# Performance work log

Hardware: AMD Instinct MI355X
Metric: run time of the kernel (lower is better)

The kernel has to match this reference:

```python
import jax, jax.numpy as jnp
import numpy as np

N = 100000   # nodes
E = 1000000  # edges
F_IN = 64    # num_node_features
H = 64       # hidden_channels
G = 64       # graphs in batch
OUT = 1


def setup_inputs() -> dict:
    key = jax.random.key(0)
    ks = jax.random.split(key, 16)
    inp = {}
    inp['x'] = jax.random.normal(ks[0], (N, F_IN), dtype=jnp.float32)
    inp['edge_index'] = jax.random.randint(ks[1], (2, E), 0, N, dtype=jnp.int64)
    inp['batch'] = jnp.sort(jax.random.randint(ks[2], (N,), 0, G, dtype=jnp.int64))
    s_in = 1.0 / np.sqrt(F_IN)
    s_h = 1.0 / np.sqrt(H)
    # GraphConv 1: in=F_IN -> H  (lin_rel has bias, lin_root has no bias)
    inp['W1r'] = jax.random.uniform(ks[3], (F_IN, H), jnp.float32, -s_in, s_in)
    inp['b1'] = jax.random.uniform(ks[4], (H,), jnp.float32, -s_in, s_in)
    inp['W1o'] = jax.random.uniform(ks[5], (F_IN, H), jnp.float32, -s_in, s_in)
    # GraphConv 2, 3: H -> H
    inp['W2r'] = jax.random.uniform(ks[6], (H, H), jnp.float32, -s_h, s_h)
    inp['b2'] = jax.random.uniform(ks[7], (H,), jnp.float32, -s_h, s_h)
    inp['W2o'] = jax.random.uniform(ks[8], (H, H), jnp.float32, -s_h, s_h)
    inp['W3r'] = jax.random.uniform(ks[9], (H, H), jnp.float32, -s_h, s_h)
    inp['b3'] = jax.random.uniform(ks[10], (H,), jnp.float32, -s_h, s_h)
    inp['W3o'] = jax.random.uniform(ks[11], (H, H), jnp.float32, -s_h, s_h)
    # PReLU slopes (num_parameters=1, init=0.25)
    inp['a1'] = jnp.array(0.25, dtype=jnp.float32)
    inp['a2'] = jnp.array(0.25, dtype=jnp.float32)
    # head
    inp['W_lin0'] = jax.random.uniform(ks[12], (H, H), jnp.float32, -s_h, s_h)
    inp['b_lin0'] = jax.random.uniform(ks[13], (H,), jnp.float32, -s_h, s_h)
    inp['W_lin1'] = jax.random.uniform(ks[14], (H, OUT), jnp.float32, -s_h, s_h)
    inp['b_lin1'] = jax.random.uniform(ks[15], (OUT,), jnp.float32, -s_h, s_h)
    return inp


def _graph_conv(x, src, dst, Wr, b, Wo):
    # PyG GraphConv, aggr='add': out_i = Wr @ (sum_{j->i} x_j) + Wo @ x_i + b.
    # Aggregate raw features first (linear commutes with sum) -> one small GEMM.
    agg = jax.ops.segment_sum(x[src], dst, num_segments=N)  # [N, d_in]
    return agg @ Wr + x @ Wo + b


def _prelu(x, a):
    return jnp.where(x >= 0, x, a * x)


def reference(x, edge_index, batch, W1r, b1, W1o, W2r, b2, W2o, W3r, b3, W3o,
              a1, a2, W_lin0, b_lin0, W_lin1, b_lin1):
    src, dst = edge_index[0], edge_index[1]
    h = _graph_conv(x, src, dst, W1r, b1, W1o)
    h = _prelu(h, a1)  # dropout is identity in eval mode
    h = _graph_conv(h, src, dst, W2r, b2, W2o)
    h = _prelu(h, a2)
    h = _graph_conv(h, src, dst, W3r, b3, W3o)
    # global_mean_pool over graph ids
    sums = jax.ops.segment_sum(h, batch, num_segments=G)            # [G, H]
    cnts = jax.ops.segment_sum(jnp.ones((N,), h.dtype), batch, num_segments=G)
    pooled = sums / jnp.maximum(cnts, 1.0)[:, None]
    out = pooled @ W_lin0 + b_lin0
    out = out @ W_lin1 + b_lin1
    return out  # [G, OUT]
```

## Files before the change

kernel.cpp:

```cpp
#include <hip/hip_runtime.h>

#define FDIM 64
#define POOL_CHUNK 64
#define ECAP 512
#define NBK_SHIFT 8
#define BCAP 4096
#define CHUNK 8192

typedef unsigned int uint32;
typedef unsigned short ushort16;
typedef __attribute__((ext_vector_type(8))) short bf8v;
typedef __attribute__((ext_vector_type(4))) float f4v;

static inline size_t align_up(size_t v) { return (v + 255) & ~(size_t)255; }

__device__ __forceinline__ float bcastf(float v, int l) {
    return __int_as_float(__builtin_amdgcn_readlane(__float_as_int(v), l));
}
__device__ __forceinline__ float bf_lo(uint32 u) { return __uint_as_float(u << 16); }
__device__ __forceinline__ float bf_hi(uint32 u) { return __uint_as_float(u & 0xFFFF0000u); }
__device__ __forceinline__ unsigned short f2bf(float f) {
    uint32 u = __float_as_uint(f);
    return (unsigned short)((u + 0x7FFFu + ((u >> 16) & 1u)) >> 16);
}
__device__ __forceinline__ float bf2f(unsigned short s) {
    return __uint_as_float(((uint32)s) << 16);
}


__global__ __launch_bounds__(256) void k_bhist(const int* __restrict__ dst,
                                               int* __restrict__ bcount, int E, int nb) {
    __shared__ int h[512];
    for (int i = threadIdx.x; i < nb; i += 256) h[i] = 0;
    __syncthreads();
    int stride = gridDim.x * blockDim.x;
    for (int e = blockIdx.x * blockDim.x + threadIdx.x; e < E; e += stride)
        atomicAdd(&h[dst[e] >> NBK_SHIFT], 1);
    __syncthreads();
    for (int i = threadIdx.x; i < nb; i += 256)
        if (h[i]) atomicAdd(&bcount[i], h[i]);
}

__global__ __launch_bounds__(512) void k_bscan(const int* __restrict__ bcount,
                                               int* __restrict__ bbase,
                                               int* __restrict__ bcursor, int nb,
                                               int* __restrict__ rowstart, int n, int E) {
    __shared__ int sh[512];
    int t = threadIdx.x;
    int v = (t < nb) ? bcount[t] : 0;
    sh[t] = v;
    __syncthreads();
    for (int off = 1; off < 512; off <<= 1) {
        int a = (t >= off) ? sh[t - off] : 0;
        __syncthreads();
        sh[t] += a;
        __syncthreads();
    }
    if (t < nb) { int ex = sh[t] - v; bbase[t] = ex; bcursor[t] = ex; }
    if (t == 0) { bbase[nb] = E; rowstart[n] = E; }
}

__global__ __launch_bounds__(512) void k_bgroup(const int* __restrict__ src,
                                                const int* __restrict__ dst,
                                                int* __restrict__ bcursor,
                                                uint32* __restrict__ ebuf, int E, int nb) {
    __shared__ uint32 sorted[CHUNK];
    __shared__ unsigned short bop[CHUNK];
    __shared__ int hist[512];
    __shared__ int gbase[512];
    __shared__ int cur[512];
    __shared__ int sh[512];
    int c0 = blockIdx.x * CHUNK;
    int cend = c0 + CHUNK; if (cend > E) cend = E;
    int cnt = cend - c0;
    int t = threadIdx.x;
    for (int i = t; i < nb; i += 512) hist[i] = 0;
    __syncthreads();
    for (int i = t; i < cnt; i += 512)
        atomicAdd(&hist[dst[c0 + i] >> NBK_SHIFT], 1);
    __syncthreads();
    int v = (t < nb) ? hist[t] : 0;
    sh[t] = v;
    __syncthreads();
    for (int off = 1; off < 512; off <<= 1) {
        int a = (t >= off) ? sh[t - off] : 0;
        __syncthreads();
        sh[t] += a;
        __syncthreads();
    }
    __syncthreads();
    if (t < nb) {
        int lofs = sh[t] - v;
        cur[t] = lofs;
        hist[t] = lofs;
        gbase[t] = v ? atomicAdd(&bcursor[t], v) : 0;
    }
    __syncthreads();
    for (int i = t; i < cnt; i += 512) {
        int d = dst[c0 + i], s = src[c0 + i];
        int b = d >> NBK_SHIFT;
        int p = atomicAdd(&cur[b], 1);
        sorted[p] = ((uint32)(d & ((1 << NBK_SHIFT) - 1)) << 24) | (uint32)s;
        bop[p] = (unsigned short)b;
    }
    __syncthreads();
    for (int i = t; i < cnt; i += 512) {
        int b = bop[i];
        ebuf[gbase[b] + (i - hist[b])] = sorted[i];
    }
}

__global__ __launch_bounds__(256) void k_blocal(const uint32* __restrict__ ebuf,
                                                const int* __restrict__ bbase,
                                                int* __restrict__ rowstart,
                                                int* __restrict__ adj, int n) {
    __shared__ uint32 raw[BCAP];
    __shared__ int srt[BCAP];
    __shared__ int hist[257];
    __shared__ int cur[256];
    int b = blockIdx.x;
    int t = threadIdx.x;
    int lo = bbase[b], hi = bbase[b + 1];
    int cnt = hi - lo;
    for (int i = t; i < 257; i += 256) hist[i] = 0;
    __syncthreads();
    if (cnt <= BCAP) {
        for (int i = t; i < cnt; i += 256) {
            uint32 v = ebuf[lo + i];
            raw[i] = v;
            atomicAdd(&hist[(v >> 24) + 1], 1);
        }
        __syncthreads();
        if (t == 0) { for (int i = 1; i <= 256; i++) hist[i] += hist[i - 1]; }
        __syncthreads();
        if (t < 256) cur[t] = hist[t];
        __syncthreads();
        for (int i = t; i < cnt; i += 256) {
            uint32 v = raw[i];
            int p = atomicAdd(&cur[v >> 24], 1);
            srt[p] = (int)(v & 0xFFFFFF);
        }
        __syncthreads();
        for (int i = t; i < cnt; i += 256) adj[lo + i] = srt[i];
    } else {
        for (int i = t; i < cnt; i += 256) {
            uint32 v = ebuf[lo + i];
            atomicAdd(&hist[(v >> 24) + 1], 1);
        }
        __syncthreads();
        if (t == 0) { for (int i = 1; i <= 256; i++) hist[i] += hist[i - 1]; }
        __syncthreads();
        if (t < 256) cur[t] = hist[t];
        __syncthreads();
        for (int i = t; i < cnt; i += 256) {
            uint32 v = ebuf[lo + i];
            int p = atomicAdd(&cur[v >> 24], 1);
            adj[lo + p] = (int)(v & 0xFFFFFF);
        }
    }
    if (t < 256) {
        int node = (b << NBK_SHIFT) + t;
        if (node < n) rowstart[node] = lo + hist[t];
    }
}


__global__ void k_cvt(const float* __restrict__ in, ushort16* __restrict__ out, long n4) {
    long i = (long)blockIdx.x * blockDim.x + threadIdx.x;
    long stride = (long)gridDim.x * blockDim.x;
    for (; i < n4; i += stride) {
        float4 v = ((const float4*)in)[i];
        uint2 o;
        o.x = (uint32)f2bf(v.x) | ((uint32)f2bf(v.y) << 16);
        o.y = (uint32)f2bf(v.z) | ((uint32)f2bf(v.w) << 16);
        ((uint2*)out)[i] = o;
    }
}


__global__ __launch_bounds__(1024) void k_layer(
    const ushort16* __restrict__ Hbf, const int* __restrict__ rowstart,
    const int* __restrict__ adj, const float* __restrict__ Wr,
    const float* __restrict__ Wo, const float* __restrict__ bias,
    const float* __restrict__ slope_p, ushort16* __restrict__ HbfOut,
    int n, int do_prelu)
{
    __shared__ unsigned short wh[64 * 128];
    __shared__ unsigned short wl[64 * 128];
    __shared__ int eidx[16][ECAP];

    for (int e = threadIdx.x; e < 64 * 128; e += 1024) {
        int nn = e >> 7;
        int k  = e & 127;
        float v = (k < 64) ? Wr[k * 64 + nn] : Wo[(k - 64) * 64 + nn];
        unsigned short hi = f2bf(v);
        unsigned short lo = f2bf(v - bf2f(hi));
        int boff = nn * 256 + ((k * 2) ^ ((nn & 7) << 4));
        wh[boff >> 1] = hi;
        wl[boff >> 1] = lo;
    }
    __syncthreads();

    int lane  = threadIdx.x & 63;
    int l15   = lane & 15;
    int kg    = lane >> 4;
    int koff  = kg * 8;
    int wslot = threadIdx.x >> 6;
    int wid  = (blockIdx.x * blockDim.x + threadIdx.x) >> 6;
    int nw   = (gridDim.x * blockDim.x) >> 6;
    int ntiles = (n + 15) >> 4;
    float slope = do_prelu ? slope_p[0] : 1.0f;
    float bv0 = bias[l15], bv1 = bias[16 + l15], bv2 = bias[32 + l15], bv3 = bias[48 + l15];

    for (int t = wid; t < ntiles; t += nw) {
        int base16 = t * 16;
        int node = base16 + l15;
        bool valid = node < n;
        int s0 = valid ? rowstart[node] : 0;
        int s1 = valid ? rowstart[node + 1] : 0;
        int ebase = __builtin_amdgcn_readlane(s0, 0);
        int eend  = __builtin_amdgcn_readlane(s1, 15);
        if (!valid) { s0 = 0; s1 = 0; }
        if (base16 + 16 > n) eend = rowstart[n];
        int ecount = eend - ebase;

        int4 su = {0, 0, 0, 0}, sv = {0, 0, 0, 0};
        if (valid) {
            const ushort16* sp = Hbf + ((long)node << 6);
            su = *(const int4*)(sp + koff);
            sv = *(const int4*)(sp + koff + 32);
        }

        int cap = ecount < ECAP ? ecount : ECAP;
        for (int i = lane; i < cap; i += 64) eidx[wslot][i] = adj[ebase + i];
        asm volatile("s_waitcnt lgkmcnt(0) vmcnt(0)" ::: "memory");

        float acc[16];
#pragma unroll
        for (int i = 0; i < 16; i++) acc[i] = 0.f;

#define ACC8(UU, BASE) \
        acc[BASE+0] += bf_lo(UU.x); acc[BASE+1] += bf_hi(UU.x); \
        acc[BASE+2] += bf_lo(UU.y); acc[BASE+3] += bf_hi(UU.y); \
        acc[BASE+4] += bf_lo(UU.z); acc[BASE+5] += bf_hi(UU.z); \
        acc[BASE+6] += bf_lo(UU.w); acc[BASE+7] += bf_hi(UU.w);

        if (ecount <= ECAP) {
            int ls0 = s0 - ebase, ls1 = s1 - ebase;
            const int* ix = eidx[wslot];
            int j = ls0;
            for (; j + 4 <= ls1; j += 4) {
                long r0 = ix[j], r1 = ix[j + 1], r2 = ix[j + 2], r3 = ix[j + 3];
                const ushort16* p0 = Hbf + (r0 << 6);
                const ushort16* p1 = Hbf + (r1 << 6);
                const ushort16* p2 = Hbf + (r2 << 6);
                const ushort16* p3 = Hbf + (r3 << 6);
                int4 u0 = *(const int4*)(p0 + koff), v0 = *(const int4*)(p0 + koff + 32);
                int4 u1 = *(const int4*)(p1 + koff), v1 = *(const int4*)(p1 + koff + 32);
                int4 u2 = *(const int4*)(p2 + koff), v2 = *(const int4*)(p2 + koff + 32);
                int4 u3 = *(const int4*)(p3 + koff), v3 = *(const int4*)(p3 + koff + 32);
                ACC8(u0, 0)  ACC8(u1, 0)  ACC8(u2, 0)  ACC8(u3, 0)
                ACC8(v0, 8)  ACC8(v1, 8)  ACC8(v2, 8)  ACC8(v3, 8)
            }
            for (; j < ls1; j++) {
                long r0 = ix[j];
                const ushort16* p0 = Hbf + (r0 << 6);
                int4 u0 = *(const int4*)(p0 + koff), v0 = *(const int4*)(p0 + koff + 32);
                ACC8(u0, 0)  ACC8(v0, 8)
            }
        } else {
            for (int e = s0; e < s1; e++) {
                long r0 = adj[e];
                const ushort16* p0 = Hbf + (r0 << 6);
                int4 u0 = *(const int4*)(p0 + koff), v0 = *(const int4*)(p0 + koff + 32);
                ACC8(u0, 0)  ACC8(v0, 8)
            }
        }
#undef ACC8

        bf8v ah[4], al[2];
#pragma unroll
        for (int kb = 0; kb < 2; kb++) {
#pragma unroll
            for (int j = 0; j < 8; j++) {
                float v = acc[kb * 8 + j];
                unsigned short h = f2bf(v);
                ah[kb][j] = (short)h;
                al[kb][j] = (short)f2bf(v - bf2f(h));
            }
        }
        ah[2] = __builtin_bit_cast(bf8v, su);
        ah[3] = __builtin_bit_cast(bf8v, sv);

        f4v C[4];
        C[0] = (f4v){bv0, bv0, bv0, bv0};
        C[1] = (f4v){bv1, bv1, bv1, bv1};
        C[2] = (f4v){bv2, bv2, bv2, bv2};
        C[3] = (f4v){bv3, bv3, bv3, bv3};

#pragma unroll
        for (int kb = 0; kb < 4; kb++) {
#pragma unroll
            for (int nt = 0; nt < 4; nt++) {
                int row = nt * 16 + l15;
                int boff = row * 256 + (((kb * 32 + kg * 8) * 2) ^ ((l15 & 7) << 4));
                bf8v bh = *(const bf8v*)((const char*)wh + boff);
                bf8v bl = *(const bf8v*)((const char*)wl + boff);
                C[nt] = __builtin_amdgcn_mfma_f32_16x16x32_bf16(ah[kb], bh, C[nt], 0, 0, 0);
                if (kb < 2)
                    C[nt] = __builtin_amdgcn_mfma_f32_16x16x32_bf16(al[kb], bh, C[nt], 0, 0, 0);
                C[nt] = __builtin_amdgcn_mfma_f32_16x16x32_bf16(ah[kb], bl, C[nt], 0, 0, 0);
            }
        }

#pragma unroll
        for (int r = 0; r < 4; r++) {
            int onode = base16 + kg * 4 + r;
            if (onode < n) {
#pragma unroll
                for (int nt = 0; nt < 4; nt++) {
                    float v = C[nt][r];
                    v = v >= 0.f ? v : slope * v;
                    HbfOut[((long)onode << 6) + nt * 16 + l15] = f2bf(v);
                }
            }
        }
    }
}


__global__ __launch_bounds__(256) void k_pool(const ushort16* __restrict__ h,
                                              const int* __restrict__ batch,
                                              float* __restrict__ sums,
                                              float* __restrict__ cnt, int n) {
    int wave = (blockIdx.x * 256 + threadIdx.x) >> 6;
    int lane = threadIdx.x & 63;
    int start = wave * POOL_CHUNK;
    if (start >= n) return;
    int end = start + POOL_CHUNK;
    if (end > n) end = n;
    int cur = batch[start];
    float acc = 0.f;
    int count = 0;
#pragma unroll 4
    for (int i = start; i < end; i++) {
        int g = batch[i];
        if (g != cur) {
            atomicAdd(&sums[cur * FDIM + lane], acc);
            if (lane == 0) atomicAdd(&cnt[cur], (float)count);
            acc = 0.f;
            count = 0;
            cur = g;
        }
        acc += bf2f(h[(long)i * FDIM + lane]);
        count++;
    }
    atomicAdd(&sums[cur * FDIM + lane], acc);
    if (lane == 0) atomicAdd(&cnt[cur], (float)count);
}


__global__ __launch_bounds__(64) void k_head(const float* __restrict__ sums,
                                             const float* __restrict__ cnt,
                                             const float* __restrict__ W0,
                                             const float* __restrict__ b0,
                                             const float* __restrict__ W1,
                                             const float* __restrict__ b1,
                                             float* __restrict__ out, int OUT) {
    int g = blockIdx.x;
    int lane = threadIdx.x;
    float c = cnt[g];
    if (c < 1.f) c = 1.f;
    float p = sums[g * FDIM + lane] / c;

    float h0 = 0.f, h1 = 0.f, h2 = 0.f, h3 = 0.f;
#pragma unroll
    for (int k = 0; k < FDIM; k += 4) {
        h0 += bcastf(p, k + 0) * W0[(k + 0) * FDIM + lane];
        h1 += bcastf(p, k + 1) * W0[(k + 1) * FDIM + lane];
        h2 += bcastf(p, k + 2) * W0[(k + 2) * FDIM + lane];
        h3 += bcastf(p, k + 3) * W0[(k + 3) * FDIM + lane];
    }
    float hid = b0[lane] + ((h0 + h1) + (h2 + h3));
    for (int o = 0; o < OUT; o++) {
        float part = hid * W1[lane * OUT + o];
#pragma unroll
        for (int m = 32; m >= 1; m >>= 1) part += __shfl_xor(part, m, 64);
        if (lane == 0) out[g * OUT + o] = part + b1[o];
    }
}

extern "C" void kernel_launch(void* const* d_in, const int* in_sizes, int n_in,
                              void* d_out, int out_size, void* d_ws, size_t ws_size,
                              hipStream_t stream) {
    const float* x     = (const float*)d_in[0];
    const int*   ei    = (const int*)d_in[1];
    const int*   batch = (const int*)d_in[2];
    const float* W1r = (const float*)d_in[3];
    const float* b1  = (const float*)d_in[4];
    const float* W1o = (const float*)d_in[5];
    const float* W2r = (const float*)d_in[6];
    const float* b2  = (const float*)d_in[7];
    const float* W2o = (const float*)d_in[8];
    const float* W3r = (const float*)d_in[9];
    const float* b3  = (const float*)d_in[10];
    const float* W3o = (const float*)d_in[11];
    const float* a1  = (const float*)d_in[12];
    const float* a2  = (const float*)d_in[13];
    const float* Wl0 = (const float*)d_in[14];
    const float* bl0 = (const float*)d_in[15];
    const float* Wl1 = (const float*)d_in[16];
    const float* bl1 = (const float*)d_in[17];

    int N = in_sizes[0] / FDIM;
    int E = in_sizes[1] / 2;
    int OUT = in_sizes[17];
    int G = out_size / OUT;
    int nb = (N + 255) >> NBK_SHIFT;

    const int* src = ei;
    const int* dst = ei + E;

    char* w = (char*)d_ws;
    int* rowstart = (int*)w;              w += align_up((size_t)(N + 1) * 4);
    int* adj      = (int*)w;              w += align_up((size_t)E * 4 + 256);
    uint32* ebuf  = (uint32*)w;           w += align_up((size_t)E * 4);
    int* bbase    = (int*)w;              w += align_up((size_t)(nb + 1) * 4);
    int* bcursor  = (int*)w;              w += align_up((size_t)nb * 4);
    ushort16* xbf = (ushort16*)w;         w += align_up((size_t)N * FDIM * 2);
    ushort16* hb1 = (ushort16*)w;         w += align_up((size_t)N * FDIM * 2);
    ushort16* hb2 = (ushort16*)w;         w += align_up((size_t)N * FDIM * 2);
    ushort16* hb3 = (ushort16*)w;         w += align_up((size_t)N * FDIM * 2);
    char* zbase   = w;
    int* bcount   = (int*)w;              w += align_up(512 * 4);
    float* sums   = (float*)w;            w += align_up((size_t)G * FDIM * 4);
    float* cnt    = (float*)w;            w += align_up((size_t)G * 4);

    hipMemsetAsync(zbase, 0, (size_t)(w - zbase), stream);

    k_bhist<<<512, 256, 0, stream>>>(dst, bcount, E, nb);
    k_bscan<<<1, 512, 0, stream>>>(bcount, bbase, bcursor, nb, rowstart, N, E);
    int nchunks = (E + CHUNK - 1) / CHUNK;
    k_bgroup<<<nchunks, 512, 0, stream>>>(src, dst, bcursor, ebuf, E, nb);
    k_blocal<<<nb, 256, 0, stream>>>(ebuf, bbase, rowstart, adj, N);

    k_cvt<<<1024, 256, 0, stream>>>(x, xbf, (long)N * FDIM / 4);

    int ntiles = (N + 15) / 16;
    int layerGrid = (ntiles + 15) / 16;
    k_layer<<<layerGrid, 1024, 0, stream>>>(xbf, rowstart, adj, W1r, W1o, b1, a1, hb1, N, 1);
    k_layer<<<layerGrid, 1024, 0, stream>>>(hb1, rowstart, adj, W2r, W2o, b2, a2, hb2, N, 1);
    k_layer<<<layerGrid, 1024, 0, stream>>>(hb2, rowstart, adj, W3r, W3o, b3, nullptr, hb3, N, 0);

    int poolWaves = (N + POOL_CHUNK - 1) / POOL_CHUNK;
    int poolGrid = (poolWaves + 3) / 4;
    k_pool<<<poolGrid, 256, 0, stream>>>(hb3, batch, sums, cnt, N);
    k_head<<<G, 64, 0, stream>>>(sums, cnt, Wl0, bl0, Wl1, bl1, (float*)d_out, OUT);
}
```

Measured before the change: 212.2 us.

## Retune block sizes, parallelize local histogram scan, shrink layer blocks

Changes k_layer to 512-thread blocks with a fixed grid of 768 and a halved shared edge-index buffer. k_bgroup moves to 1024-thread blocks, and the serial single-thread prefix sum in k_blocal becomes a parallel Hillis-Steele scan. The pool chunk size is also halved. The aim is better occupancy and less serialized work in the preprocessing kernels, at the cost of more barriers in the scans. A fixed grid for the layer kernel relies on its grid-stride loop to cover all tiles.

```diff
diff --git a/kernel.cpp b/kernel.cpp
--- a/kernel.cpp
+++ b/kernel.cpp
@@ -1,7 +1,7 @@
 #include <hip/hip_runtime.h>
 
 #define FDIM 64
-#define POOL_CHUNK 64
+#define POOL_CHUNK 32
 #define ECAP 512
 #define NBK_SHIFT 8
 #define BCAP 4096
@@ -60,10 +60,10 @@
     if (t == 0) { bbase[nb] = E; rowstart[n] = E; }
 }
 
-__global__ __launch_bounds__(512) void k_bgroup(const int* __restrict__ src,
-                                                const int* __restrict__ dst,
-                                                int* __restrict__ bcursor,
-                                                uint32* __restrict__ ebuf, int E, int nb) {
+__global__ __launch_bounds__(1024) void k_bgroup(const int* __restrict__ src,
+                                                 const int* __restrict__ dst,
+                                                 int* __restrict__ bcursor,
+                                                 uint32* __restrict__ ebuf, int E, int nb) {
     __shared__ uint32 sorted[CHUNK];
     __shared__ unsigned short bop[CHUNK];
     __shared__ int hist[512];
@@ -74,21 +74,20 @@
     int cend = c0 + CHUNK; if (cend > E) cend = E;
     int cnt = cend - c0;
     int t = threadIdx.x;
-    for (int i = t; i < nb; i += 512) hist[i] = 0;
-    __syncthreads();
-    for (int i = t; i < cnt; i += 512)
+    for (int i = t; i < nb; i += 1024) hist[i] = 0;
+    __syncthreads();
+    for (int i = t; i < cnt; i += 1024)
         atomicAdd(&hist[dst[c0 + i] >> NBK_SHIFT], 1);
     __syncthreads();
-    int v = (t < nb) ? hist[t] : 0;
-    sh[t] = v;
+    int v = 0;
+    if (t < 512) { v = (t < nb) ? hist[t] : 0; sh[t] = v; }
     __syncthreads();
     for (int off = 1; off < 512; off <<= 1) {
-        int a = (t >= off) ? sh[t - off] : 0;
-        __syncthreads();
-        sh[t] += a;
-        __syncthreads();
-    }
-    __syncthreads();
+        int a = (t >= off && t < 512) ? sh[t - off] : 0;
+        __syncthreads();
+        if (t < 512) sh[t] += a;
+        __syncthreads();
+    }
     if (t < nb) {
         int lofs = sh[t] - v;
         cur[t] = lofs;
@@ -96,7 +95,7 @@
         gbase[t] = v ? atomicAdd(&bcursor[t], v) : 0;
     }
     __syncthreads();
-    for (int i = t; i < cnt; i += 512) {
+    for (int i = t; i < cnt; i += 1024) {
         int d = dst[c0 + i], s = src[c0 + i];
         int b = d >> NBK_SHIFT;
         int p = atomicAdd(&cur[b], 1);
@@ -104,7 +103,7 @@
         bop[p] = (unsigned short)b;
     }
     __syncthreads();
-    for (int i = t; i < cnt; i += 512) {
+    for (int i = t; i < cnt; i += 1024) {
         int b = bop[i];
         ebuf[gbase[b] + (i - hist[b])] = sorted[i];
     }
@@ -131,8 +130,16 @@
             atomicAdd(&hist[(v >> 24) + 1], 1);
         }
         __syncthreads();
-        if (t == 0) { for (int i = 1; i <= 256; i++) hist[i] += hist[i - 1]; }
-        __syncthreads();
+        {
+            int v = hist[t + 1];
+            for (int off = 1; off < 256; off <<= 1) {
+                int a = (t >= off) ? hist[t + 1 - off] : 0;
+                __syncthreads();
+                hist[t + 1] += a;
+                __syncthreads();
+                (void)v;
+            }
+        }
         if (t < 256) cur[t] = hist[t];
         __syncthreads();
         for (int i = t; i < cnt; i += 256) {
@@ -148,8 +155,16 @@
             atomicAdd(&hist[(v >> 24) + 1], 1);
         }
         __syncthreads();
-        if (t == 0) { for (int i = 1; i <= 256; i++) hist[i] += hist[i - 1]; }
-        __syncthreads();
+        {
+            int v = hist[t + 1];
+            for (int off = 1; off < 256; off <<= 1) {
+                int a = (t >= off) ? hist[t + 1 - off] : 0;
+                __syncthreads();
+                hist[t + 1] += a;
+                __syncthreads();
+                (void)v;
+            }
+        }
         if (t < 256) cur[t] = hist[t];
         __syncthreads();
         for (int i = t; i < cnt; i += 256) {
@@ -178,7 +193,7 @@
 }
 
 
-__global__ __launch_bounds__(1024) void k_layer(
+__global__ __launch_bounds__(512) void k_layer(
     const ushort16* __restrict__ Hbf, const int* __restrict__ rowstart,
     const int* __restrict__ adj, const float* __restrict__ Wr,
     const float* __restrict__ Wo, const float* __restrict__ bias,
@@ -187,9 +202,9 @@
 {
     __shared__ unsigned short wh[64 * 128];
     __shared__ unsigned short wl[64 * 128];
-    __shared__ int eidx[16][ECAP];
-
-    for (int e = threadIdx.x; e < 64 * 128; e += 1024) {
+    __shared__ int eidx[8][ECAP];
+
+    for (int e = threadIdx.x; e < 64 * 128; e += 512) {
         int nn = e >> 7;
         int k  = e & 127;
         float v = (k < 64) ? Wr[k * 64 + nn] : Wo[(k - 64) * 64 + nn];
@@ -441,16 +456,15 @@
     k_bhist<<<512, 256, 0, stream>>>(dst, bcount, E, nb);
     k_bscan<<<1, 512, 0, stream>>>(bcount, bbase, bcursor, nb, rowstart, N, E);
     int nchunks = (E + CHUNK - 1) / CHUNK;
-    k_bgroup<<<nchunks, 512, 0, stream>>>(src, dst, bcursor, ebuf, E, nb);
+    k_bgroup<<<nchunks, 1024, 0, stream>>>(src, dst, bcursor, ebuf, E, nb);
     k_blocal<<<nb, 256, 0, stream>>>(ebuf, bbase, rowstart, adj, N);
 
     k_cvt<<<1024, 256, 0, stream>>>(x, xbf, (long)N * FDIM / 4);
 
-    int ntiles = (N + 15) / 16;
-    int layerGrid = (ntiles + 15) / 16;
-    k_layer<<<layerGrid, 1024, 0, stream>>>(xbf, rowstart, adj, W1r, W1o, b1, a1, hb1, N, 1);
-    k_layer<<<layerGrid, 1024, 0, stream>>>(hb1, rowstart, adj, W2r, W2o, b2, a2, hb2, N, 1);
-    k_layer<<<layerGrid, 1024, 0, stream>>>(hb2, rowstart, adj, W3r, W3o, b3, nullptr, hb3, N, 0);
+    int layerGrid = 768;
+    k_layer<<<layerGrid, 512, 0, stream>>>(xbf, rowstart, adj, W1r, W1o, b1, a1, hb1, N, 1);
+    k_layer<<<layerGrid, 512, 0, stream>>>(hb1, rowstart, adj, W2r, W2o, b2, a2, hb2, N, 1);
+    k_layer<<<layerGrid, 512, 0, stream>>>(hb2, rowstart, adj, W3r, W3o, b3, nullptr, hb3, N, 0);
 
     int poolWaves = (N + POOL_CHUNK - 1) / POOL_CHUNK;
     int poolGrid = (poolWaves + 3) / 4;
```

New measurement: 218.1 us. +2.8%, slower.
